# Kernel tuning notes

Measured on AMD Instinct MI355X. Metric: run time of the kernel, lower is better.

The kernel has to match this reference:

```python
import jax, jax.numpy as jnp
import numpy as np

H = 768      # hidden_size
NH = 12      # num_heads
HD = H // NH # head_dim = 64


def setup_inputs() -> dict:
    key = jax.random.key(0)
    k1, k2, k3 = jax.random.split(key, 3)
    x = jax.random.normal(k1, (4, 2048, H), dtype=jnp.float32)
    # nn.Linear weights are [out, in]; we store transposed [in, out] for x @ W
    w_qkv = jax.random.normal(k2, (H, 3 * H), dtype=jnp.float32) * (1.0 / np.sqrt(H))
    w_out = jax.random.normal(k3, (H, H), dtype=jnp.float32) * (1.0 / np.sqrt(H))
    return {"x": x, "w_qkv": w_qkv, "w_out": w_out}


def reference(x, w_qkv, w_out):
    B, S, _ = x.shape
    qkv = (x @ w_qkv).reshape(B, S, 3, NH, HD)
    qkv = jnp.transpose(qkv, (2, 0, 3, 1, 4))  # [3, B, NH, S, HD]
    q, k, v = qkv[0], qkv[1], qkv[2]
    scale = 1.0 / np.sqrt(HD)
    scores = jnp.einsum('bhqd,bhkd->bhqk', q, k) * scale  # [B,NH,S,S]
    causal = jnp.tril(jnp.ones((S, S), dtype=bool))
    scores = jnp.where(causal, scores, jnp.finfo(scores.dtype).min)
    attn = jax.nn.softmax(scores, axis=-1)
    out = jnp.einsum('bhqk,bhkd->bhqd', attn, v)          # [B,NH,S,HD]
    out = jnp.transpose(out, (0, 2, 1, 3)).reshape(B, S, H)
    return out @ w_out
```

## Files before the change

kernel.cpp:

```cpp
#include <hip/hip_runtime.h>
#include <type_traits>

#define S_LEN 2048
#define HID   768
#define NHEAD 12
#define HDIM  64
#define BATCH 4

typedef __attribute__((ext_vector_type(4))) float float4v;
typedef __attribute__((ext_vector_type(8))) short short8;
typedef __attribute__((ext_vector_type(4))) short short4v;
typedef __attribute__((ext_vector_type(2))) int int2v;

__device__ __forceinline__ short f2b(float f) {
  unsigned u = __float_as_uint(f);
  u += 0x7fff + ((u >> 16) & 1);
  return (short)(u >> 16);
}

__device__ __forceinline__ unsigned pkbf(float a, float b) {
#if __has_builtin(__builtin_amdgcn_cvt_pk_bf16_f32)
  typedef __attribute__((ext_vector_type(2))) __bf16 bf2;
  bf2 r = __builtin_amdgcn_cvt_pk_bf16_f32(a, b);
  return *(unsigned*)&r;
#else
  return ((unsigned)(unsigned short)f2b(a)) |
         (((unsigned)(unsigned short)f2b(b)) << 16);
#endif
}

__device__ __forceinline__ float fexp2(float x) {
#if __has_builtin(__builtin_amdgcn_exp2f)
  return __builtin_amdgcn_exp2f(x);
#else
  return __expf(x * 0.69314718056f);
#endif
}

__device__ __forceinline__ void g2l16(const short* g, short* l) {
  __builtin_amdgcn_global_load_lds(
      (const __attribute__((address_space(1))) void*)g,
      (__attribute__((address_space(3))) void*)l, 16, 0, 0);
}

__global__ __launch_bounds__(256) void prepass(const float* __restrict__ x,
                                               const float* __restrict__ w_qkv,
                                               const float* __restrict__ w_out,
                                               short* __restrict__ xb,
                                               short* __restrict__ wqkvT,
                                               short* __restrict__ woutT) {
  __shared__ float tile[64][65];
  const int blk = blockIdx.x;
  if (blk < 3072) {
    int i = blk * 2048 + threadIdx.x * 8;
    float4v a = *(const float4v*)&x[i];
    float4v b = *(const float4v*)&x[i + 4];
    short8 o;
#pragma unroll
    for (int j = 0; j < 4; j++) { o[j] = f2b(a[j]); o[j + 4] = f2b(b[j]); }
    *(short8*)&xb[i] = o;
    return;
  }
  const float* W; short* WT; int N_, scaleN, idx;
  if (blk < 3504) { idx = blk - 3072; W = w_qkv; WT = wqkvT; N_ = 3 * HID; scaleN = HID; }
  else            { idx = blk - 3504; W = w_out; WT = woutT; N_ = HID;     scaleN = 0;  }
  const int nblk = N_ / 64;
  const int n0 = (idx % nblk) * 64, k0 = (idx / nblk) * 64;
  const int tx = threadIdx.x & 63, ty = threadIdx.x >> 6;
#pragma unroll
  for (int r = 0; r < 16; r++) {
    int row = r * 4 + ty;
    tile[row][tx] = W[(size_t)(k0 + row) * N_ + n0 + tx];
  }
  __syncthreads();
#pragma unroll
  for (int r = 0; r < 16; r++) {
    int row = r * 4 + ty;
    float sc = (n0 + row < scaleN) ? 0.18033688011f : 1.0f;
    WT[(size_t)(n0 + row) * HID + k0 + tx] = f2b(tile[tx][row] * sc);
  }
}

template <int OUT>
__global__ __launch_bounds__(256) void gemm_bt(const short* __restrict__ A,
                                               const short* __restrict__ Bt,
                                               float* __restrict__ Cf,
                                               short* __restrict__ Cq,
                                               short* __restrict__ vT,
                                               int M, int N, int K) {
  __shared__ __align__(16) short As[2][128 * 32];
  __shared__ __align__(16) short Bs[2][128 * 32];
  const int tid = threadIdx.x;
  const int w = tid >> 6, lane = tid & 63;
  const int quad = lane >> 4, lm = lane & 15;

  const int gx = gridDim.x;
  const int nwg = gx * gridDim.y;
  int flat = blockIdx.y * gx + blockIdx.x;
  if ((nwg & 7) == 0) flat = (flat & 7) * (nwg >> 3) + (flat >> 3);
  const int m0 = (flat / gx) * 128, n0 = (flat % gx) * 128;
  const int mo = (w & 1) * 64, no = (w >> 1) * 64;

  float4v acc[4][4];
#pragma unroll
  for (int i = 0; i < 4; i++)
#pragma unroll
    for (int j = 0; j < 4; j++) acc[i][j] = (float4v)0.0f;

  const int srow = w * 32 + (lane >> 2);
  const int scol = ((lane & 3) ^ ((lane >> 3) & 3)) * 8;
  const short* Ag = A + (size_t)(m0 + srow) * K + scol;
  const short* Bg = Bt + (size_t)(n0 + srow) * K + scol;

  const int qsw8 = (quad ^ ((lm >> 1) & 3)) * 8;

  for (int kb = 0; kb < K; kb += 64) {
#pragma unroll
    for (int s = 0; s < 2; s++) {
      short* Al = &As[s][(w * 32) * 32];
      short* Bl = &Bs[s][(w * 32) * 32];
      g2l16(Ag + kb + s * 32, Al);
      g2l16(Ag + kb + s * 32 + (size_t)16 * K, Al + 16 * 32);
      g2l16(Bg + kb + s * 32, Bl);
      g2l16(Bg + kb + s * 32 + (size_t)16 * K, Bl + 16 * 32);
    }
    __syncthreads();

#pragma unroll
    for (int s = 0; s < 2; s++) {
      short8 af[4], bf[4];
#pragma unroll
      for (int i = 0; i < 4; i++)
        af[i] = *(const short8*)&As[s][(mo + i * 16 + lm) * 32 + qsw8];
#pragma unroll
      for (int j = 0; j < 4; j++)
        bf[j] = *(const short8*)&Bs[s][(no + j * 16 + lm) * 32 + qsw8];
#pragma unroll
      for (int i = 0; i < 4; i++)
#pragma unroll
        for (int j = 0; j < 4; j++) {
          if constexpr (OUT == 2)
            acc[i][j] = __builtin_amdgcn_mfma_f32_16x16x32_bf16(bf[j], af[i], acc[i][j], 0, 0, 0);
          else
            acc[i][j] = __builtin_amdgcn_mfma_f32_16x16x32_bf16(af[i], bf[j], acc[i][j], 0, 0, 0);
        }
    }
    __syncthreads();
  }

  if constexpr (OUT == 0) {
#pragma unroll
    for (int i = 0; i < 4; i++)
#pragma unroll
      for (int j = 0; j < 4; j++)
#pragma unroll
        for (int r = 0; r < 4; r++)
          Cf[(size_t)(m0 + mo + i * 16 + quad * 4 + r) * N + n0 + no + j * 16 + lm] =
              acc[i][j][r];
  } else if constexpr (OUT == 1) {
#pragma unroll
    for (int i = 0; i < 4; i++)
#pragma unroll
      for (int j = 0; j < 4; j++)
#pragma unroll
        for (int r = 0; r < 4; r++)
          Cq[(size_t)(m0 + mo + i * 16 + quad * 4 + r) * (2 * HID) + n0 + no + j * 16 + lm] =
              f2b(acc[i][j][r]);
  } else {
    const int b = m0 >> 11;
#pragma unroll
    for (int i = 0; i < 4; i++) {
      const int sG = (m0 & 2047) + mo + i * 16 + lm;
#pragma unroll
      for (int j = 0; j < 4; j++) {
#pragma unroll
        for (int r = 0; r < 4; r++) {
          int col = n0 + no + j * 16 + quad * 4 + r;
          int h = col >> 6, d = col & 63;
          vT[((size_t)(b * NHEAD + h) * HDIM + d) * S_LEN + sG] = f2b(acc[i][j][r]);
        }
      }
    }
  }
}

__global__ __launch_bounds__(256) void attn_mfma(const short* __restrict__ qk,
                                                 const short* __restrict__ vT,
                                                 short* __restrict__ attnout) {
  __shared__ __align__(16) short Ks[2][64 * 64];
  __shared__ __align__(16) short Vt[2][64 * 64];
  __shared__ __align__(16) short Ps[4][16 * 64];

  const int tid = threadIdx.x;
  const int w = tid >> 6, lane = tid & 63;
  const int quad = lane >> 4, lm = lane & 15;
  const int bh = blockIdx.x;
  const int qt = 31 - blockIdx.y;
  const int b = bh / NHEAD, h = bh % NHEAD;

  short8 aq[2];
#pragma unroll
  for (int kb = 0; kb < 2; kb++)
    aq[kb] = *(const short8*)&qk[(size_t)(b * S_LEN + qt * 64 + w * 16 + lm) * (2 * HID) +
                                 h * HDIM + kb * 32 + quad * 8];

  const float4v z4 = (float4v)0.0f;
  short8 one8;
#pragma unroll
  for (int j = 0; j < 8; j++) one8[j] = (short)0x3F80;

  const size_t kbase = (size_t)(b * S_LEN) * (2 * HID) + HID + h * HDIM;
  const size_t vbase = (size_t)(b * NHEAD + h) * HDIM * S_LEN;
  const short* kptr[2];
  const short* vptr[2];
#pragma unroll
  for (int i = 0; i < 2; i++) {
    int c = (w * 2 + i) * 64 + lane;
    int row = c >> 3, slot = c & 7;
    int q8 = slot ^ (row & 7);
    int key = 4 * (row & 15) + (row >> 4);
    kptr[i] = qk + kbase + (size_t)key * (2 * HID) + q8 * 8;
    vptr[i] = vT + vbase + (size_t)row * S_LEN + q8 * 8;
  }

#define ISSUE(BUF)                                                    \
  {                                                                   \
    _Pragma("unroll") for (int i = 0; i < 2; i++) {                   \
      g2l16(kptr[i], &Ks[BUF][(w * 2 + i) * 512]);                    \
      g2l16(vptr[i], &Vt[BUF][(w * 2 + i) * 512]);                    \
      kptr[i] += 64 * 2 * HID;                                        \
      vptr[i] += 64;                                                  \
    }                                                                 \
  }

  const int swx = (lm & 7) << 4;
  const int loff0 = (quad * 16) ^ swx;
  const int loff1 = (64 + quad * 16) ^ swx;
  const int rowK = lm << 7;
  const char* KsB = (const char*)&Ks[0][0];
  const char* VtB = (const char*)&Vt[0][0];
  const char* PsW = (const char*)&Ps[w][0];
  const char* pread0 = PsW + rowK + loff0;
  const char* pread1 = PsW + rowK + loff1;
  char* pswa[4];
#pragma unroll
  for (int r = 0; r < 4; r++) {
    int rowp = quad * 4 + r;
    pswa[r] = (char*)PsW + (rowp << 7) + ((lm * 8) ^ ((rowp & 7) << 4));
  }

  float4v o_acc[4];
#pragma unroll
  for (int nt = 0; nt < 4; nt++) o_acc[nt] = (float4v)0.0f;
  float4v o1 = (float4v)0.0f;

  const int ktmax = qt + 1;
  int cur = 0;

  ISSUE(0);

  for (int kt = 0; kt < ktmax; kt++) {
    asm volatile("s_waitcnt vmcnt(0)" ::: "memory");
    __syncthreads();
    if (kt + 1 < ktmax) ISSUE(cur ^ 1);

    const int coff = cur << 13;
    const char* kB0 = KsB + coff + rowK + loff0;
    const char* kB1 = KsB + coff + rowK + loff1;
    const char* vB0 = VtB + coff + rowK + loff0;
    const char* vB1 = VtB + coff + rowK + loff1;

    float4v s_acc[4];
    __builtin_amdgcn_s_setprio(1);
#pragma unroll
    for (int nt = 0; nt < 4; nt++) {
      short8 bk = *(const short8*)(kB0 + nt * 2048);
      s_acc[nt] = __builtin_amdgcn_mfma_f32_16x16x32_bf16(aq[0], bk, z4, 0, 0, 0);
    }
#pragma unroll
    for (int nt = 0; nt < 4; nt++) {
      short8 bk = *(const short8*)(kB1 + nt * 2048);
      s_acc[nt] = __builtin_amdgcn_mfma_f32_16x16x32_bf16(aq[1], bk, s_acc[nt], 0, 0, 0);
    }
    __builtin_amdgcn_s_setprio(0);

    const bool diag = (kt == qt);
#pragma unroll
    for (int r = 0; r < 4; r++) {
      float e[4];
#pragma unroll
      for (int nt = 0; nt < 4; nt++) {
        float v = fexp2(s_acc[nt][r]);
        if (diag && (4 * lm + nt > w * 16 + quad * 4 + r)) v = 0.0f;
        e[nt] = v;
      }
      int2v p2 = {(int)pkbf(e[0], e[1]), (int)pkbf(e[2], e[3])};
      *(int2v*)pswa[r] = p2;
    }

    __builtin_amdgcn_s_setprio(1);
#pragma unroll
    for (int kb = 0; kb < 2; kb++) {
      short8 ap = *(const short8*)(kb ? pread1 : pread0);
      const char* vB = kb ? vB1 : vB0;
      o1 = __builtin_amdgcn_mfma_f32_16x16x32_bf16(ap, one8, o1, 0, 0, 0);
#pragma unroll
      for (int nt = 0; nt < 4; nt++) {
        short8 bv = *(const short8*)(vB + nt * 2048);
        o_acc[nt] = __builtin_amdgcn_mfma_f32_16x16x32_bf16(ap, bv, o_acc[nt], 0, 0, 0);
      }
    }
    __builtin_amdgcn_s_setprio(0);

    cur ^= 1;
  }

#pragma unroll
  for (int r = 0; r < 4; r++) {
    float inv = 1.0f / o1[r];
    int rowg = b * S_LEN + qt * 64 + w * 16 + quad * 4 + r;
#pragma unroll
    for (int nt = 0; nt < 4; nt++)
      attnout[(size_t)rowg * HID + h * HDIM + nt * 16 + lm] =
          f2b(o_acc[nt][r] * inv);
  }
#undef ISSUE
}

extern "C" void kernel_launch(void* const* d_in, const int* in_sizes, int n_in,
                              void* d_out, int out_size, void* d_ws, size_t ws_size,
                              hipStream_t stream) {
  const float* x     = (const float*)d_in[0];
  const float* w_qkv = (const float*)d_in[1];
  const float* w_out = (const float*)d_in[2];
  float* out = (float*)d_out;

  const int M = BATCH * S_LEN;
  short* qk     = (short*)d_ws;
  short* attn   = qk + (size_t)M * 2 * HID;
  short* vT     = attn + (size_t)M * HID;
  short* xb     = vT + (size_t)M * HID;
  short* wqkvT  = xb + (size_t)M * HID;
  short* woutT  = wqkvT + (size_t)(3 * HID) * HID;

  prepass<<<3648, 256, 0, stream>>>(x, w_qkv, w_out, xb, wqkvT, woutT);

  gemm_bt<1><<<dim3(2 * HID / 128, M / 128), 256, 0, stream>>>(
      xb, wqkvT, nullptr, qk, nullptr, M, 2 * HID, HID);
  gemm_bt<2><<<dim3(HID / 128, M / 128), 256, 0, stream>>>(
      xb, wqkvT + (size_t)(2 * HID) * HID, nullptr, nullptr, vT, M, HID, HID);
  attn_mfma<<<dim3(BATCH * NHEAD, 32), 256, 0, stream>>>(qk, vT, attn);
  gemm_bt<0><<<dim3(HID / 128, M / 128), 256, 0, stream>>>(
      attn, woutT, out, nullptr, nullptr, M, HID, HID);
}
```

Measured before the change: 196.2 us.

## Triple-buffer GEMM LDS staging with prefetch two k-tiles ahead

Replaces the load-all-then-compute double-slot loop in the bf16 GEMM with a three-buffer software pipeline. Global-to-LDS copies for k-tile kt+2 are issued while k-tile kt is computed. A partial s_waitcnt vmcnt plus a single barrier per 32-wide k-step replaces the two barriers per 64-wide step. This aims to hide global load latency behind MFMA work, at the cost of 50% more LDS per block, which may lower occupancy. The loop also assumes the k-tile count is a multiple of three.

```diff
diff --git a/kernel.cpp b/kernel.cpp
--- a/kernel.cpp
+++ b/kernel.cpp
@@ -88,8 +88,8 @@
                                                short* __restrict__ Cq,
                                                short* __restrict__ vT,
                                                int M, int N, int K) {
-  __shared__ __align__(16) short As[2][128 * 32];
-  __shared__ __align__(16) short Bs[2][128 * 32];
+  __shared__ __align__(16) short As[3][128 * 32];
+  __shared__ __align__(16) short Bs[3][128 * 32];
   const int tid = threadIdx.x;
   const int w = tid >> 6, lane = tid & 63;
   const int quad = lane >> 4, lm = lane & 15;
@@ -114,39 +114,54 @@
 
   const int qsw8 = (quad ^ ((lm >> 1) & 3)) * 8;
 
-  for (int kb = 0; kb < K; kb += 64) {
-#pragma unroll
-    for (int s = 0; s < 2; s++) {
-      short* Al = &As[s][(w * 32) * 32];
-      short* Bl = &Bs[s][(w * 32) * 32];
-      g2l16(Ag + kb + s * 32, Al);
-      g2l16(Ag + kb + s * 32 + (size_t)16 * K, Al + 16 * 32);
-      g2l16(Bg + kb + s * 32, Bl);
-      g2l16(Bg + kb + s * 32 + (size_t)16 * K, Bl + 16 * 32);
-    }
-    __syncthreads();
-
-#pragma unroll
-    for (int s = 0; s < 2; s++) {
-      short8 af[4], bf[4];
-#pragma unroll
-      for (int i = 0; i < 4; i++)
-        af[i] = *(const short8*)&As[s][(mo + i * 16 + lm) * 32 + qsw8];
-#pragma unroll
-      for (int j = 0; j < 4; j++)
-        bf[j] = *(const short8*)&Bs[s][(no + j * 16 + lm) * 32 + qsw8];
-#pragma unroll
-      for (int i = 0; i < 4; i++)
-#pragma unroll
-        for (int j = 0; j < 4; j++) {
-          if constexpr (OUT == 2)
-            acc[i][j] = __builtin_amdgcn_mfma_f32_16x16x32_bf16(bf[j], af[i], acc[i][j], 0, 0, 0);
-          else
-            acc[i][j] = __builtin_amdgcn_mfma_f32_16x16x32_bf16(af[i], bf[j], acc[i][j], 0, 0, 0);
-        }
-    }
-    __syncthreads();
-  }
+  const int nkt = K / 32;
+
+#define STAGE(KT, B)                                          \
+  {                                                           \
+    const short* ag = Ag + (KT) * 32;                         \
+    const short* bg = Bg + (KT) * 32;                         \
+    short* al = &As[B][(w * 32) * 32];                        \
+    short* bl = &Bs[B][(w * 32) * 32];                        \
+    g2l16(ag, al);                                            \
+    g2l16(ag + (size_t)16 * K, al + 16 * 32);                 \
+    g2l16(bg, bl);                                            \
+    g2l16(bg + (size_t)16 * K, bl + 16 * 32);                 \
+  }
+
+#define ITER(KT, CB, SB)                                                     \
+  {                                                                          \
+    if ((KT) + 1 < nkt)                                                      \
+      asm volatile("s_waitcnt vmcnt(4)" ::: "memory");                       \
+    else                                                                     \
+      asm volatile("s_waitcnt vmcnt(0)" ::: "memory");                       \
+    __builtin_amdgcn_s_barrier();                                            \
+    asm volatile("" ::: "memory");                                           \
+    if ((KT) + 2 < nkt) STAGE((KT) + 2, SB);                                 \
+    short8 af[4], bf[4];                                                     \
+    _Pragma("unroll") for (int i = 0; i < 4; i++)                            \
+      af[i] = *(const short8*)&As[CB][(mo + i * 16 + lm) * 32 + qsw8];       \
+    _Pragma("unroll") for (int j = 0; j < 4; j++)                            \
+      bf[j] = *(const short8*)&Bs[CB][(no + j * 16 + lm) * 32 + qsw8];       \
+    _Pragma("unroll") for (int i = 0; i < 4; i++)                            \
+      _Pragma("unroll") for (int j = 0; j < 4; j++) {                        \
+        if constexpr (OUT == 2)                                              \
+          acc[i][j] =                                                        \
+              __builtin_amdgcn_mfma_f32_16x16x32_bf16(bf[j], af[i], acc[i][j], 0, 0, 0); \
+        else                                                                 \
+          acc[i][j] =                                                        \
+              __builtin_amdgcn_mfma_f32_16x16x32_bf16(af[i], bf[j], acc[i][j], 0, 0, 0); \
+      }                                                                      \
+  }
+
+  STAGE(0, 0);
+  STAGE(1, 1);
+  for (int kt = 0; kt < nkt; kt += 3) {
+    ITER(kt + 0, 0, 2);
+    ITER(kt + 1, 1, 0);
+    ITER(kt + 2, 2, 1);
+  }
+#undef ITER
+#undef STAGE
 
   if constexpr (OUT == 0) {
 #pragma unroll
```

After: 205.6 us. +4.8%, slower.

## Keep softmax probabilities in registers by computing transposed scores

Applied to the files above, without the earlier changes.

Swaps the MFMA operand order so the QK^T tile comes out transposed (keys along rows per lane). The key-to-LDS-row mapping is permuted so each lane's accumulator values can be packed directly into the A operand of the PV MFMA. This removes the per-wave shared-memory staging buffer for P along with its writes, reads and the associated LDS latency. The causal mask index is adjusted to match the new layout, which risks subtle indexing errors.

```diff
diff --git a/kernel.cpp b/kernel.cpp
--- a/kernel.cpp
+++ b/kernel.cpp
@@ -11,6 +11,7 @@
 typedef __attribute__((ext_vector_type(8))) short short8;
 typedef __attribute__((ext_vector_type(4))) short short4v;
 typedef __attribute__((ext_vector_type(2))) int int2v;
+typedef __attribute__((ext_vector_type(4))) int int4v;
 
 __device__ __forceinline__ short f2b(float f) {
   unsigned u = __float_as_uint(f);
@@ -189,7 +190,6 @@
                                                  short* __restrict__ attnout) {
   __shared__ __align__(16) short Ks[2][64 * 64];
   __shared__ __align__(16) short Vt[2][64 * 64];
-  __shared__ __align__(16) short Ps[4][16 * 64];
 
   const int tid = threadIdx.x;
   const int w = tid >> 6, lane = tid & 63;
@@ -218,7 +218,8 @@
     int c = (w * 2 + i) * 64 + lane;
     int row = c >> 3, slot = c & 7;
     int q8 = slot ^ (row & 7);
-    int key = 4 * (row & 15) + (row >> 4);
+    int ra = row & 15, nt = row >> 4;
+    int key = 8 * (ra >> 2) + 2 * (ra & 3) + (nt & 1) + 32 * (nt >> 1);
     kptr[i] = qk + kbase + (size_t)key * (2 * HID) + q8 * 8;
     vptr[i] = vT + vbase + (size_t)row * S_LEN + q8 * 8;
   }
@@ -239,15 +240,6 @@
   const int rowK = lm << 7;
   const char* KsB = (const char*)&Ks[0][0];
   const char* VtB = (const char*)&Vt[0][0];
-  const char* PsW = (const char*)&Ps[w][0];
-  const char* pread0 = PsW + rowK + loff0;
-  const char* pread1 = PsW + rowK + loff1;
-  char* pswa[4];
-#pragma unroll
-  for (int r = 0; r < 4; r++) {
-    int rowp = quad * 4 + r;
-    pswa[r] = (char*)PsW + (rowp << 7) + ((lm * 8) ^ ((rowp & 7) << 4));
-  }
 
   float4v o_acc[4];
 #pragma unroll
@@ -275,40 +267,48 @@
 #pragma unroll
     for (int nt = 0; nt < 4; nt++) {
       short8 bk = *(const short8*)(kB0 + nt * 2048);
-      s_acc[nt] = __builtin_amdgcn_mfma_f32_16x16x32_bf16(aq[0], bk, z4, 0, 0, 0);
+      s_acc[nt] = __builtin_amdgcn_mfma_f32_16x16x32_bf16(bk, aq[0], z4, 0, 0, 0);
     }
 #pragma unroll
     for (int nt = 0; nt < 4; nt++) {
       short8 bk = *(const short8*)(kB1 + nt * 2048);
-      s_acc[nt] = __builtin_amdgcn_mfma_f32_16x16x32_bf16(aq[1], bk, s_acc[nt], 0, 0, 0);
+      s_acc[nt] = __builtin_amdgcn_mfma_f32_16x16x32_bf16(bk, aq[1], s_acc[nt], 0, 0, 0);
     }
     __builtin_amdgcn_s_setprio(0);
 
     const bool diag = (kt == qt);
-#pragma unroll
-    for (int r = 0; r < 4; r++) {
-      float e[4];
-#pragma unroll
-      for (int nt = 0; nt < 4; nt++) {
+    float e[4][4];
+#pragma unroll
+    for (int nt = 0; nt < 4; nt++)
+#pragma unroll
+      for (int r = 0; r < 4; r++) {
         float v = fexp2(s_acc[nt][r]);
-        if (diag && (4 * lm + nt > w * 16 + quad * 4 + r)) v = 0.0f;
-        e[nt] = v;
+        if (diag && (8 * quad + 2 * r + (nt & 1) + 32 * (nt >> 1) > w * 16 + lm)) v = 0.0f;
+        e[nt][r] = v;
       }
-      int2v p2 = {(int)pkbf(e[0], e[1]), (int)pkbf(e[2], e[3])};
-      *(int2v*)pswa[r] = p2;
-    }
+
+    int4v p0i = {(int)pkbf(e[0][0], e[1][0]), (int)pkbf(e[0][1], e[1][1]),
+                 (int)pkbf(e[0][2], e[1][2]), (int)pkbf(e[0][3], e[1][3])};
+    int4v p1i = {(int)pkbf(e[2][0], e[3][0]), (int)pkbf(e[2][1], e[3][1]),
+                 (int)pkbf(e[2][2], e[3][2]), (int)pkbf(e[2][3], e[3][3])};
+    union UU { int4v i; short8 s; };
+    UU u0, u1;
+    u0.i = p0i;
+    u1.i = p1i;
+    short8 ap0 = u0.s, ap1 = u1.s;
 
     __builtin_amdgcn_s_setprio(1);
-#pragma unroll
-    for (int kb = 0; kb < 2; kb++) {
-      short8 ap = *(const short8*)(kb ? pread1 : pread0);
-      const char* vB = kb ? vB1 : vB0;
-      o1 = __builtin_amdgcn_mfma_f32_16x16x32_bf16(ap, one8, o1, 0, 0, 0);
-#pragma unroll
-      for (int nt = 0; nt < 4; nt++) {
-        short8 bv = *(const short8*)(vB + nt * 2048);
-        o_acc[nt] = __builtin_amdgcn_mfma_f32_16x16x32_bf16(ap, bv, o_acc[nt], 0, 0, 0);
-      }
+    o1 = __builtin_amdgcn_mfma_f32_16x16x32_bf16(ap0, one8, o1, 0, 0, 0);
+#pragma unroll
+    for (int nt = 0; nt < 4; nt++) {
+      short8 bv = *(const short8*)(vB0 + nt * 2048);
+      o_acc[nt] = __builtin_amdgcn_mfma_f32_16x16x32_bf16(ap0, bv, o_acc[nt], 0, 0, 0);
+    }
+    o1 = __builtin_amdgcn_mfma_f32_16x16x32_bf16(ap1, one8, o1, 0, 0, 0);
+#pragma unroll
+    for (int nt = 0; nt < 4; nt++) {
+      short8 bv = *(const short8*)(vB1 + nt * 2048);
+      o_acc[nt] = __builtin_amdgcn_mfma_f32_16x16x32_bf16(ap1, bv, o_acc[nt], 0, 0, 0);
     }
     __builtin_amdgcn_s_setprio(0);
 
```

After: 191.8 us. 1.02x faster.
